# Kernel tuning notes

Measured on AMD Instinct MI355X. Metric: run time of the kernel, lower is better.

Reference implementation:

```python
import jax, jax.numpy as jnp
import numpy as np

SEQ, BATCH, IN, H = 512, 2048, 4, 50


def setup_inputs() -> dict:
    key = jax.random.key(0)
    ks = jax.random.split(key, 12)
    k = 1.0 / np.sqrt(H)  # torch LSTM/Linear init scale
    u = lambda kk, shape: jax.random.uniform(kk, shape, jnp.float32, -k, k)
    return {
        "x": jax.random.normal(ks[0], (SEQ, BATCH, IN), jnp.float32),
        "w_ih1": u(ks[1], (4 * H, IN)),
        "w_hh1": u(ks[2], (4 * H, H)),
        "b_ih1": u(ks[3], (4 * H,)),
        "b_hh1": u(ks[4], (4 * H,)),
        "w_ih2": u(ks[5], (4 * H, H)),
        "w_hh2": u(ks[6], (4 * H, H)),
        "b_ih2": u(ks[7], (4 * H,)),
        "b_hh2": u(ks[8], (4 * H,)),
        "w_fc": u(ks[9], (1, H)),
        "b_fc": u(ks[10], (1,)),
    }


def _lstm(x, w_ih, w_hh, b_ih, b_hh):
    """Single-layer LSTM, torch gate order (i, f, g, o). x: [S,B,D] -> h: [S,B,H]."""
    h_dim = w_hh.shape[1]
    # Precompute input contribution for all timesteps at once: [S,B,4H]
    xg = jnp.einsum('sbd,gd->sbg', x, w_ih) + b_ih + b_hh

    def step(carry, xg_t):
        h, c = carry
        gates = xg_t + h @ w_hh.T  # [B,4H]
        i, f, g, o = jnp.split(gates, 4, axis=-1)
        c = jax.nn.sigmoid(f) * c + jax.nn.sigmoid(i) * jnp.tanh(g)
        h = jax.nn.sigmoid(o) * jnp.tanh(c)
        return (h, c), h

    b = x.shape[1]
    h0 = jnp.zeros((b, h_dim), x.dtype)
    (_, _), hs = jax.lax.scan(step, (h0, h0), xg)
    return hs  # [S,B,H]


def reference(x, w_ih1, w_hh1, b_ih1, b_hh1, w_ih2, w_hh2, b_ih2, b_hh2, w_fc, b_fc):
    h1 = jax.nn.relu(_lstm(x, w_ih1, w_hh1, b_ih1, b_hh1))
    h2 = jax.nn.relu(_lstm(h1, w_ih2, w_hh2, b_ih2, b_hh2))
    return h2 @ w_fc.T + b_fc  # [S,B,1]
```

## Files before the change

kernel.cpp:

```cpp
#include <hip/hip_runtime.h>
#include <cstdint>

#define SEQ 512
#define BATCH 2048
#define HID 50
#define BB 8
#define NTHR 1024
#define NBLK (BATCH / BB)
#define NT 13
#define S1H 80
#define S2H 144

typedef _Float16 f16;
typedef _Float16 v8h __attribute__((ext_vector_type(8)));
typedef float    v4f __attribute__((ext_vector_type(4)));

#if __has_builtin(__builtin_amdgcn_exp2f)
#define EXP2F(x) __builtin_amdgcn_exp2f(x)
#else
#define EXP2F(x) exp2f(x)
#endif
#define RCPF(x) __builtin_amdgcn_rcpf(x)
#define LOG2E 1.44269504f
#define MFMA(A,B,C) __builtin_amdgcn_mfma_f32_16x16x32_f16(A, B, C, 0, 0, 0)


__global__ __launch_bounds__(NTHR, 1) void lstm2_fused(
    const float* __restrict__ x,
    const float* __restrict__ w_ih1, const float* __restrict__ w_hh1,
    const float* __restrict__ b_ih1, const float* __restrict__ b_hh1,
    const float* __restrict__ w_ih2, const float* __restrict__ w_hh2,
    const float* __restrict__ b_ih2, const float* __restrict__ b_hh2,
    const float* __restrict__ w_fc, const float* __restrict__ b_fc,
    float* __restrict__ out)
{
    __shared__ __align__(16) f16 u1h[2][BB * S1H];
    __shared__ __align__(16) f16 u2h[2][BB * S2H];
    __shared__ float fcw[2][8][64];
    __shared__ __align__(16) f16 xl[SEQ][BB * 4];
    __shared__ __align__(16) float outb[SEQ][BB];

    const int tid  = threadIdx.x;
    const int wv   = tid >> 6;
    const int lane = tid & 63;
    const int mb   = lane & 15;
    const int q    = lane >> 4;
    const int bbase = blockIdx.x * BB;

    const bool grpB = (wv >= 8);
    const int  wa   = grpB ? (15 - wv) : wv;
    const bool heavy = (wa < NT - 8);

    const bool hiHalf = (mb >= 8);
    const int  myt    = hiHalf ? (wa + 8) : wa;
    const int  u_me   = myt * 4 + q;
    const bool valid_upd = (myt < NT) && (u_me < HID);
    const int  b_me   = mb & 7;

    const int   gidx = mb & 3;
    const float sc   = (gidx == 2) ? (2.0f * LOG2E) : (-LOG2E);

    v8h Af[2][4];
#pragma unroll
    for (int i = 0; i < 2; ++i) {
        const int tt = wa + 8 * i;
        const bool tv = (tt < NT);
        const int ru = tt * 4 + (mb >> 2);
        const bool rv = tv && (ru < HID);
        const int R = gidx * HID + ru;
        if (!grpB) {
#pragma unroll
            for (int kt = 0; kt < 2; ++kt) {
                v8h f;
#pragma unroll
                for (int j = 0; j < 8; ++j) {
                    const int kk = kt * 32 + q * 8 + j;
                    float v = 0.0f;
                    if (rv) {
                        if (kk < 4) v = w_ih1[R * 4 + kk];
                        else if (kk < 54) v = w_hh1[R * HID + (kk - 4)];
                    }
                    f[j] = (f16)(v * sc);
                }
                Af[i][kt] = f;
            }
        } else {
#pragma unroll
            for (int kt = 0; kt < 4; ++kt) {
                v8h f;
#pragma unroll
                for (int j = 0; j < 8; ++j) {
                    const int kk = kt * 32 + q * 8 + j;
                    float v = 0.0f;
                    if (rv) {
                        if (kk < HID) v = w_ih2[R * HID + kk];
                        else if (kk < 2 * HID) v = w_hh2[R * HID + (kk - HID)];
                    }
                    f[j] = (f16)(v * sc);
                }
                Af[i][kt] = f;
            }
        }
    }

    v4f bias0 = {0.f, 0.f, 0.f, 0.f}, bias1 = {0.f, 0.f, 0.f, 0.f};
#pragma unroll
    for (int r = 0; r < 4; ++r) {
        const float scr = (r == 2) ? (2.0f * LOG2E) : (-LOG2E);
        const int u0 = wa * 4 + q;
        const int u1t = (wa + 8) * 4 + q;
        const float* bi = grpB ? b_ih2 : b_ih1;
        const float* bh = grpB ? b_hh2 : b_hh1;
        if (u0 < HID) bias0[r] = (bi[r * HID + u0] + bh[r * HID + u0]) * scr;
        if ((wa + 8) < NT && u1t < HID)
            bias1[r] = (bi[r * HID + u1t] + bh[r * HID + u1t]) * scr;
    }
    const float wfc_me = (grpB && valid_upd) ? w_fc[u_me] : 0.0f;
    const float bfc = b_fc[0];
    float c_me = 0.0f;

    for (int idx = tid; idx < 2 * BB * S1H; idx += NTHR) ((f16*)u1h)[idx] = (f16)0.0f;
    for (int idx = tid; idx < 2 * BB * S2H; idx += NTHR) ((f16*)u2h)[idx] = (f16)0.0f;
    ((float*)fcw)[tid] = 0.0f;
    for (int i = tid; i < SEQ * BB; i += NTHR) {
        const int t = i >> 3, b = i & 7;
        const float4 v = *reinterpret_cast<const float4*>(
            x + ((size_t)t * BATCH + bbase + b) * 4);
        f16 p[4] = {(f16)v.x, (f16)v.y, (f16)v.z, (f16)v.w};
        *reinterpret_cast<uint2*>(&xl[t][b * 4]) = *reinterpret_cast<uint2*>(p);
    }
    __syncthreads();
    if (tid < BB) {
        *reinterpret_cast<uint2*>(&u1h[0][tid * S1H]) =
            *reinterpret_cast<const uint2*>(&xl[0][tid * 4]);
    }
    __syncthreads();

    if (heavy) __builtin_amdgcn_s_setprio(1);

    const f16* u1rp[2] = {u1h[0] + b_me * S1H, u1h[1] + b_me * S1H};
    const f16* u2rp[2] = {u2h[0] + b_me * S2H, u2h[1] + b_me * S2H};
    f16* u1wp[2] = {u1h[0] + b_me * S1H, u1h[1] + b_me * S1H};
    f16* u2wp[2] = {u2h[0] + b_me * S2H, u2h[1] + b_me * S2H};

    auto body = [&](int s, int pr, int pn) __attribute__((always_inline)) {
        if (!grpB) {
            const f16* u1r = u1rp[pr];
            const v8h B0 = *reinterpret_cast<const v8h*>(&u1r[q * 8]);
            const v8h B1 = *reinterpret_cast<const v8h*>(&u1r[32 + q * 8]);
            v4f a0 = bias0;
            a0 = MFMA(Af[0][0], B0, a0);
            a0 = MFMA(Af[0][1], B1, a0);
            v4f m = a0;
            if (heavy) {
                v4f a1 = bias1;
                a1 = MFMA(Af[1][0], B0, a1);
                a1 = MFMA(Af[1][1], B1, a1);
                if (hiHalf) m = a1;
            }
            const float A  = 1.0f + EXP2F(m[0]);
            const float F  = 1.0f + EXP2F(m[1]);
            const float Bv = 1.0f + EXP2F(m[2]);
            const float C  = 1.0f + EXP2F(m[3]);
            const float AB = A * Bv;
            c_me = (c_me * AB + (Bv - 2.0f) * F) * RCPF(F * AB);
            const float D = 1.0f + EXP2F(c_me * (2.0f * LOG2E));
            const float h1v = (D - 2.0f) * RCPF(C * D);
            if (valid_upd) {
                u1wp[pn][4 + u_me] = (f16)h1v;
                u2wp[pr][u_me] = (f16)fmaxf(h1v, 0.0f);
            }
            if (wv == 6 && s >= 2) {
                float v = 0.0f;
#pragma unroll
                for (int k2 = 0; k2 < 8; ++k2) v += fcw[pn][k2][lane];
                v += __shfl_xor(v, 8);
                v += __shfl_xor(v, 16);
                v += __shfl_xor(v, 32);
                if (lane < BB) outb[s - 2][lane] = v + bfc;
            }
        } else {
            if (wv == 8 && lane < BB) {
                const int tn = (s + 1 < SEQ) ? s + 1 : SEQ - 1;
                *reinterpret_cast<uint2*>(&u1h[pn][lane * S1H]) =
                    *reinterpret_cast<const uint2*>(&xl[tn][lane * 4]);
            }
            const f16* u2r = u2rp[pn];
            const v8h C0 = *reinterpret_cast<const v8h*>(&u2r[q * 8]);
            const v8h C1 = *reinterpret_cast<const v8h*>(&u2r[32 + q * 8]);
            const v8h C2 = *reinterpret_cast<const v8h*>(&u2r[64 + q * 8]);
            const v8h C3 = *reinterpret_cast<const v8h*>(&u2r[96 + q * 8]);
            v4f a0 = bias0;
            a0 = MFMA(Af[0][0], C0, a0);
            a0 = MFMA(Af[0][1], C1, a0);
            a0 = MFMA(Af[0][2], C2, a0);
            a0 = MFMA(Af[0][3], C3, a0);
            v4f m = a0;
            if (heavy) {
                v4f a1 = bias1;
                a1 = MFMA(Af[1][0], C0, a1);
                a1 = MFMA(Af[1][1], C1, a1);
                a1 = MFMA(Af[1][2], C2, a1);
                a1 = MFMA(Af[1][3], C3, a1);
                if (hiHalf) m = a1;
            }
            const float A  = 1.0f + EXP2F(m[0]);
            const float F  = 1.0f + EXP2F(m[1]);
            const float Bv = 1.0f + EXP2F(m[2]);
            const float C  = 1.0f + EXP2F(m[3]);
            const float AB = A * Bv;
            const float cn = (c_me * AB + (Bv - 2.0f) * F) * RCPF(F * AB);
            const float D = 1.0f + EXP2F(cn * (2.0f * LOG2E));
            const float h2v = (D - 2.0f) * RCPF(C * D);
            float p = 0.0f;
            if (s >= 1) {
                c_me = cn;
                if (valid_upd) u2wp[pr][HID + u_me] = (f16)h2v;
                p = fmaxf(h2v, 0.0f) * wfc_me;
            }
            fcw[pr][wv - 8][lane] = p;
        }
        __syncthreads();
    };

#pragma unroll 1
    for (int s = 0; s < SEQ + 2; s += 2) {
        body(s, 0, 1);
        body(s + 1, 1, 0);
    }

    {
        const int i = tid;
        const int t = i >> 1, hb = (i & 1) * 4;
        *reinterpret_cast<float4*>(out + (size_t)t * BATCH + bbase + hb) =
            *reinterpret_cast<const float4*>(&outb[t][hb]);
    }
}

extern "C" void kernel_launch(void* const* d_in, const int* in_sizes, int n_in,
                              void* d_out, int out_size, void* d_ws, size_t ws_size,
                              hipStream_t stream) {
    const float* X    = (const float*)d_in[0];
    const float* Wih1 = (const float*)d_in[1];
    const float* Whh1 = (const float*)d_in[2];
    const float* Bih1 = (const float*)d_in[3];
    const float* Bhh1 = (const float*)d_in[4];
    const float* Wih2 = (const float*)d_in[5];
    const float* Whh2 = (const float*)d_in[6];
    const float* Bih2 = (const float*)d_in[7];
    const float* Bhh2 = (const float*)d_in[8];
    const float* Wfc  = (const float*)d_in[9];
    const float* Bfc  = (const float*)d_in[10];
    float* out = (float*)d_out;

    lstm2_fused<<<dim3(NBLK), dim3(NTHR), 0, stream>>>(
        X, Wih1, Whh1, Bih1, Bhh1, Wih2, Whh2, Bih2, Bhh2, Wfc, Bfc, out);
}
```

Before: 332.7 us.

## Deepen layer-2 pipeline with quad-buffered state and prefetched ReLU operands

Layer 2 now runs one step further behind layer 1, and its state buffer becomes four-deep. This lets the ReLU(h1) half of the layer-2 input be loaded from LDS one step early into registers. The layer-2 recurrent weights are realigned to a 64-column offset so each K half is a separate MFMA chain, and layer 1 also splits its accumulation into two independent chains that are summed. The goal is to shorten the serial MFMA dependency chain and hide LDS latency on the per-step critical path, at the cost of two extra steps, more LDS and more registers.

```diff
diff --git a/kernel.cpp b/kernel.cpp
--- a/kernel.cpp
+++ b/kernel.cpp
@@ -10,6 +10,7 @@
 #define NT 13
 #define S1H 80
 #define S2H 144
+#define NSTEP 516
 
 typedef _Float16 f16;
 typedef _Float16 v8h __attribute__((ext_vector_type(8)));
@@ -35,7 +36,7 @@
     float* __restrict__ out)
 {
     __shared__ __align__(16) f16 u1h[2][BB * S1H];
-    __shared__ __align__(16) f16 u2h[2][BB * S2H];
+    __shared__ __align__(16) f16 u2h[4][BB * S2H];
     __shared__ float fcw[2][8][64];
     __shared__ __align__(16) f16 xl[SEQ][BB * 4];
     __shared__ __align__(16) float outb[SEQ][BB];
@@ -94,7 +95,7 @@
                     float v = 0.0f;
                     if (rv) {
                         if (kk < HID) v = w_ih2[R * HID + kk];
-                        else if (kk < 2 * HID) v = w_hh2[R * HID + (kk - HID)];
+                        else if (kk >= 64 && kk < 64 + HID) v = w_hh2[R * HID + (kk - 64)];
                     }
                     f[j] = (f16)(v * sc);
                 }
@@ -118,9 +119,10 @@
     const float wfc_me = (grpB && valid_upd) ? w_fc[u_me] : 0.0f;
     const float bfc = b_fc[0];
     float c_me = 0.0f;
+    const v4f zf = {0.f, 0.f, 0.f, 0.f};
 
     for (int idx = tid; idx < 2 * BB * S1H; idx += NTHR) ((f16*)u1h)[idx] = (f16)0.0f;
-    for (int idx = tid; idx < 2 * BB * S2H; idx += NTHR) ((f16*)u2h)[idx] = (f16)0.0f;
+    for (int idx = tid; idx < 4 * BB * S2H; idx += NTHR) ((f16*)u2h)[idx] = (f16)0.0f;
     ((float*)fcw)[tid] = 0.0f;
     for (int i = tid; i < SEQ * BB; i += NTHR) {
         const int t = i >> 3, b = i & 7;
@@ -138,25 +140,29 @@
 
     if (heavy) __builtin_amdgcn_s_setprio(1);
 
-    const f16* u1rp[2] = {u1h[0] + b_me * S1H, u1h[1] + b_me * S1H};
-    const f16* u2rp[2] = {u2h[0] + b_me * S2H, u2h[1] + b_me * S2H};
-    f16* u1wp[2] = {u1h[0] + b_me * S1H, u1h[1] + b_me * S1H};
-    f16* u2wp[2] = {u2h[0] + b_me * S2H, u2h[1] + b_me * S2H};
-
-    auto body = [&](int s, int pr, int pn) __attribute__((always_inline)) {
+    const int off_rd1 = b_me * S1H + q * 8;
+    const int off_rd2 = b_me * S2H + q * 8;
+    const int off_w_h1   = b_me * S1H + 4 + u_me;
+    const int off_w_relu = b_me * S2H + u_me;
+    const int off_w_h2   = b_me * S2H + 64 + u_me;
+
+    v8h c0f = {}; v8h c1f = {};
+
+    auto body = [&](int s, int ph) __attribute__((always_inline)) {
+        const int pr = ph & 1, pn = pr ^ 1;
         if (!grpB) {
-            const f16* u1r = u1rp[pr];
-            const v8h B0 = *reinterpret_cast<const v8h*>(&u1r[q * 8]);
-            const v8h B1 = *reinterpret_cast<const v8h*>(&u1r[32 + q * 8]);
-            v4f a0 = bias0;
-            a0 = MFMA(Af[0][0], B0, a0);
-            a0 = MFMA(Af[0][1], B1, a0);
-            v4f m = a0;
+            const f16* u1r = &u1h[pr][off_rd1];
+            const v8h B0 = *reinterpret_cast<const v8h*>(u1r);
+            const v8h B1 = *reinterpret_cast<const v8h*>(u1r + 32);
+            v4f a0  = MFMA(Af[0][0], B0, bias0);
+            v4f a0b = MFMA(Af[0][1], B1, zf);
+            v4f m;
             if (heavy) {
-                v4f a1 = bias1;
-                a1 = MFMA(Af[1][0], B0, a1);
-                a1 = MFMA(Af[1][1], B1, a1);
-                if (hiHalf) m = a1;
+                v4f a1  = MFMA(Af[1][0], B0, bias1);
+                v4f a1b = MFMA(Af[1][1], B1, zf);
+                m = (hiHalf ? a1 : a0) + (hiHalf ? a1b : a0b);
+            } else {
+                m = a0 + a0b;
             }
             const float A  = 1.0f + EXP2F(m[0]);
             const float F  = 1.0f + EXP2F(m[1]);
@@ -167,17 +173,17 @@
             const float D = 1.0f + EXP2F(c_me * (2.0f * LOG2E));
             const float h1v = (D - 2.0f) * RCPF(C * D);
             if (valid_upd) {
-                u1wp[pn][4 + u_me] = (f16)h1v;
-                u2wp[pr][u_me] = (f16)fmaxf(h1v, 0.0f);
-            }
-            if (wv == 6 && s >= 2) {
+                u1h[pn][off_w_h1] = (f16)h1v;
+                u2h[(ph + 2) & 3][off_w_relu] = (f16)fmaxf(h1v, 0.0f);
+            }
+            if (wv == 6 && s >= 3 && s < SEQ + 3) {
                 float v = 0.0f;
 #pragma unroll
                 for (int k2 = 0; k2 < 8; ++k2) v += fcw[pn][k2][lane];
                 v += __shfl_xor(v, 8);
                 v += __shfl_xor(v, 16);
                 v += __shfl_xor(v, 32);
-                if (lane < BB) outb[s - 2][lane] = v + bfc;
+                if (lane < BB) outb[s - 3][lane] = v + bfc;
             }
         } else {
             if (wv == 8 && lane < BB) {
@@ -185,24 +191,27 @@
                 *reinterpret_cast<uint2*>(&u1h[pn][lane * S1H]) =
                     *reinterpret_cast<const uint2*>(&xl[tn][lane * 4]);
             }
-            const f16* u2r = u2rp[pn];
-            const v8h C0 = *reinterpret_cast<const v8h*>(&u2r[q * 8]);
-            const v8h C1 = *reinterpret_cast<const v8h*>(&u2r[32 + q * 8]);
-            const v8h C2 = *reinterpret_cast<const v8h*>(&u2r[64 + q * 8]);
-            const v8h C3 = *reinterpret_cast<const v8h*>(&u2r[96 + q * 8]);
-            v4f a0 = bias0;
-            a0 = MFMA(Af[0][0], C0, a0);
-            a0 = MFMA(Af[0][1], C1, a0);
-            a0 = MFMA(Af[0][2], C2, a0);
-            a0 = MFMA(Af[0][3], C3, a0);
-            v4f m = a0;
+            const f16* u2r = &u2h[ph][off_rd2];
+            const v8h C2 = *reinterpret_cast<const v8h*>(u2r + 64);
+            const v8h C3 = *reinterpret_cast<const v8h*>(u2r + 96);
+            v4f a0 = MFMA(Af[0][0], c0f, bias0);
+            a0 = MFMA(Af[0][1], c1f, a0);
+            v4f a0b = MFMA(Af[0][2], C2, zf);
+            a0b = MFMA(Af[0][3], C3, a0b);
+            v4f m;
             if (heavy) {
-                v4f a1 = bias1;
-                a1 = MFMA(Af[1][0], C0, a1);
-                a1 = MFMA(Af[1][1], C1, a1);
-                a1 = MFMA(Af[1][2], C2, a1);
-                a1 = MFMA(Af[1][3], C3, a1);
-                if (hiHalf) m = a1;
+                v4f a1 = MFMA(Af[1][0], c0f, bias1);
+                a1 = MFMA(Af[1][1], c1f, a1);
+                v4f a1b = MFMA(Af[1][2], C2, zf);
+                a1b = MFMA(Af[1][3], C3, a1b);
+                m = (hiHalf ? a1 : a0) + (hiHalf ? a1b : a0b);
+            } else {
+                m = a0 + a0b;
+            }
+            {
+                const f16* u2p = &u2h[(ph + 1) & 3][off_rd2];
+                c0f = *reinterpret_cast<const v8h*>(u2p);
+                c1f = *reinterpret_cast<const v8h*>(u2p + 32);
             }
             const float A  = 1.0f + EXP2F(m[0]);
             const float F  = 1.0f + EXP2F(m[1]);
@@ -213,9 +222,9 @@
             const float D = 1.0f + EXP2F(cn * (2.0f * LOG2E));
             const float h2v = (D - 2.0f) * RCPF(C * D);
             float p = 0.0f;
-            if (s >= 1) {
+            if (s >= 2 && s < SEQ + 2) {
                 c_me = cn;
-                if (valid_upd) u2wp[pr][HID + u_me] = (f16)h2v;
+                if (valid_upd) u2h[(ph + 1) & 3][off_w_h2] = (f16)h2v;
                 p = fmaxf(h2v, 0.0f) * wfc_me;
             }
             fcw[pr][wv - 8][lane] = p;
@@ -224,9 +233,11 @@
     };
 
 #pragma unroll 1
-    for (int s = 0; s < SEQ + 2; s += 2) {
-        body(s, 0, 1);
-        body(s + 1, 1, 0);
+    for (int s = 0; s < NSTEP; s += 4) {
+        body(s, 0);
+        body(s + 1, 1);
+        body(s + 2, 2);
+        body(s + 3, 3);
     }
 
     {
```

New measurement: 365.6 us. 1.1x slower.

## Deepen layer-2 input pipeline with 4-slot ring buffer and register prefetch

Applied to the files above, without the earlier changes.

Layer 2's input half (relu of h1) is now written two steps ahead into a 4-slot shared ring buffer. The layer-2 waves prefetch that half into registers one step early, so only the recurrent h2 half is read from LDS in the critical step. The h2 section is realigned to offset 64, with the weight packing changed to match. The pipeline lag grows by one step, which adds iterations, more LDS, and a held-over register pair per wave, in exchange for fewer LDS reads before the MFMAs.

```diff
diff --git a/kernel.cpp b/kernel.cpp
--- a/kernel.cpp
+++ b/kernel.cpp
@@ -10,6 +10,8 @@
 #define NT 13
 #define S1H 80
 #define S2H 144
+#define SL2 (BB * S2H)
+#define NSTEP 516
 
 typedef _Float16 f16;
 typedef _Float16 v8h __attribute__((ext_vector_type(8)));
@@ -35,7 +37,7 @@
     float* __restrict__ out)
 {
     __shared__ __align__(16) f16 u1h[2][BB * S1H];
-    __shared__ __align__(16) f16 u2h[2][BB * S2H];
+    __shared__ __align__(16) f16 u2h[4][SL2];
     __shared__ float fcw[2][8][64];
     __shared__ __align__(16) f16 xl[SEQ][BB * 4];
     __shared__ __align__(16) float outb[SEQ][BB];
@@ -94,7 +96,7 @@
                     float v = 0.0f;
                     if (rv) {
                         if (kk < HID) v = w_ih2[R * HID + kk];
-                        else if (kk < 2 * HID) v = w_hh2[R * HID + (kk - HID)];
+                        else if (kk >= 64 && kk < 64 + HID) v = w_hh2[R * HID + (kk - 64)];
                     }
                     f[j] = (f16)(v * sc);
                 }
@@ -120,7 +122,7 @@
     float c_me = 0.0f;
 
     for (int idx = tid; idx < 2 * BB * S1H; idx += NTHR) ((f16*)u1h)[idx] = (f16)0.0f;
-    for (int idx = tid; idx < 2 * BB * S2H; idx += NTHR) ((f16*)u2h)[idx] = (f16)0.0f;
+    for (int idx = tid; idx < 4 * SL2; idx += NTHR) ((f16*)u2h)[idx] = (f16)0.0f;
     ((float*)fcw)[tid] = 0.0f;
     for (int i = tid; i < SEQ * BB; i += NTHR) {
         const int t = i >> 3, b = i & 7;
@@ -138,12 +140,19 @@
 
     if (heavy) __builtin_amdgcn_s_setprio(1);
 
+    f16* const u2f = &u2h[0][0];
+    const int off_rd2    = b_me * S2H + q * 8;
+    const int off_w_relu = b_me * S2H + u_me;
+    const int off_w_h2   = b_me * S2H + 64 + u_me;
     const f16* u1rp[2] = {u1h[0] + b_me * S1H, u1h[1] + b_me * S1H};
-    const f16* u2rp[2] = {u2h[0] + b_me * S2H, u2h[1] + b_me * S2H};
     f16* u1wp[2] = {u1h[0] + b_me * S1H, u1h[1] + b_me * S1H};
-    f16* u2wp[2] = {u2h[0] + b_me * S2H, u2h[1] + b_me * S2H};
+
+    v8h c0f = {}; v8h c1f = {};
 
     auto body = [&](int s, int pr, int pn) __attribute__((always_inline)) {
+        const int sl_rd = (s & 3) * SL2;
+        const int sl_n1 = ((s + 1) & 3) * SL2;
+        const int sl_n2 = ((s + 2) & 3) * SL2;
         if (!grpB) {
             const f16* u1r = u1rp[pr];
             const v8h B0 = *reinterpret_cast<const v8h*>(&u1r[q * 8]);
@@ -168,16 +177,16 @@
             const float h1v = (D - 2.0f) * RCPF(C * D);
             if (valid_upd) {
                 u1wp[pn][4 + u_me] = (f16)h1v;
-                u2wp[pr][u_me] = (f16)fmaxf(h1v, 0.0f);
-            }
-            if (wv == 6 && s >= 2) {
+                u2f[sl_n2 + off_w_relu] = (f16)fmaxf(h1v, 0.0f);
+            }
+            if (wv == 6 && s >= 3 && s < SEQ + 3) {
                 float v = 0.0f;
 #pragma unroll
                 for (int k2 = 0; k2 < 8; ++k2) v += fcw[pn][k2][lane];
                 v += __shfl_xor(v, 8);
                 v += __shfl_xor(v, 16);
                 v += __shfl_xor(v, 32);
-                if (lane < BB) outb[s - 2][lane] = v + bfc;
+                if (lane < BB) outb[s - 3][lane] = v + bfc;
             }
         } else {
             if (wv == 8 && lane < BB) {
@@ -185,25 +194,27 @@
                 *reinterpret_cast<uint2*>(&u1h[pn][lane * S1H]) =
                     *reinterpret_cast<const uint2*>(&xl[tn][lane * 4]);
             }
-            const f16* u2r = u2rp[pn];
-            const v8h C0 = *reinterpret_cast<const v8h*>(&u2r[q * 8]);
-            const v8h C1 = *reinterpret_cast<const v8h*>(&u2r[32 + q * 8]);
-            const v8h C2 = *reinterpret_cast<const v8h*>(&u2r[64 + q * 8]);
-            const v8h C3 = *reinterpret_cast<const v8h*>(&u2r[96 + q * 8]);
+            const f16* rd = u2f + sl_rd + off_rd2;
+            const v8h C2 = *reinterpret_cast<const v8h*>(rd + 64);
+            const v8h C3 = *reinterpret_cast<const v8h*>(rd + 96);
+            const f16* pf = u2f + sl_n1 + off_rd2;
+            const v8h nc0 = *reinterpret_cast<const v8h*>(pf);
+            const v8h nc1 = *reinterpret_cast<const v8h*>(pf + 32);
             v4f a0 = bias0;
-            a0 = MFMA(Af[0][0], C0, a0);
-            a0 = MFMA(Af[0][1], C1, a0);
+            a0 = MFMA(Af[0][0], c0f, a0);
+            a0 = MFMA(Af[0][1], c1f, a0);
             a0 = MFMA(Af[0][2], C2, a0);
             a0 = MFMA(Af[0][3], C3, a0);
             v4f m = a0;
             if (heavy) {
                 v4f a1 = bias1;
-                a1 = MFMA(Af[1][0], C0, a1);
-                a1 = MFMA(Af[1][1], C1, a1);
+                a1 = MFMA(Af[1][0], c0f, a1);
+                a1 = MFMA(Af[1][1], c1f, a1);
                 a1 = MFMA(Af[1][2], C2, a1);
                 a1 = MFMA(Af[1][3], C3, a1);
                 if (hiHalf) m = a1;
             }
+            c0f = nc0; c1f = nc1;
             const float A  = 1.0f + EXP2F(m[0]);
             const float F  = 1.0f + EXP2F(m[1]);
             const float Bv = 1.0f + EXP2F(m[2]);
@@ -213,9 +224,9 @@
             const float D = 1.0f + EXP2F(cn * (2.0f * LOG2E));
             const float h2v = (D - 2.0f) * RCPF(C * D);
             float p = 0.0f;
-            if (s >= 1) {
+            if (s >= 2 && s < SEQ + 2) {
                 c_me = cn;
-                if (valid_upd) u2wp[pr][HID + u_me] = (f16)h2v;
+                if (valid_upd) u2f[sl_n1 + off_w_h2] = (f16)h2v;
                 p = fmaxf(h2v, 0.0f) * wfc_me;
             }
             fcw[pr][wv - 8][lane] = p;
@@ -224,7 +235,7 @@
     };
 
 #pragma unroll 1
-    for (int s = 0; s < SEQ + 2; s += 2) {
+    for (int s = 0; s < NSTEP; s += 2) {
         body(s, 0, 1);
         body(s + 1, 1, 0);
     }
```

Result: no change. 335.0 us (+0.7%).
